# Kernel optimization log

Measured on AMD Instinct MI355X. Metric: run time of the kernel, lower is better.

## Reference

```python
import jax, jax.numpy as jnp
import numpy as np

N_NODES = 50000
N_EDGES = 400000
DIM = 64
HEADS = 8
NUM_GRAPHS = 64
OUT_DIM = 32
NEG_SLOPE = 0.2
EPS = 1e-5


def setup_inputs() -> dict:
    key = jax.random.key(0)
    ks = jax.random.split(key, 20)
    inp = {
        "x": jax.random.normal(ks[0], (N_NODES, DIM), dtype=jnp.float32),
        "edge_index": jax.random.randint(ks[1], (2, N_EDGES), 0, N_NODES, dtype=jnp.int64),
        "batch": jnp.sort(jax.random.randint(ks[2], (N_NODES,), 0, NUM_GRAPHS, dtype=jnp.int64)),
    }
    s = 0.05
    # GATConv layer 1 (in=DIM, out=DIM per head, heads=HEADS, concat=False)
    inp["W1"] = jax.random.normal(ks[3], (DIM, HEADS * DIM), dtype=jnp.float32) * s
    inp["a_src1"] = jax.random.normal(ks[4], (HEADS, DIM), dtype=jnp.float32) * s
    inp["a_dst1"] = jax.random.normal(ks[5], (HEADS, DIM), dtype=jnp.float32) * s
    inp["b1"] = jnp.zeros((DIM,), dtype=jnp.float32)
    inp["ln1_w"] = jnp.ones((DIM,), dtype=jnp.float32)
    inp["ln1_b"] = jnp.zeros((DIM,), dtype=jnp.float32)
    # GATConv layer 2
    inp["W2"] = jax.random.normal(ks[6], (DIM, HEADS * DIM), dtype=jnp.float32) * s
    inp["a_src2"] = jax.random.normal(ks[7], (HEADS, DIM), dtype=jnp.float32) * s
    inp["a_dst2"] = jax.random.normal(ks[8], (HEADS, DIM), dtype=jnp.float32) * s
    inp["b2"] = jnp.zeros((DIM,), dtype=jnp.float32)
    inp["ln2_w"] = jnp.ones((DIM,), dtype=jnp.float32)
    inp["ln2_b"] = jnp.zeros((DIM,), dtype=jnp.float32)
    # DownStream head
    inp["Wh"] = jax.random.normal(ks[9], (DIM, OUT_DIM), dtype=jnp.float32) * s
    inp["bh"] = jnp.zeros((OUT_DIM,), dtype=jnp.float32)
    return inp


def _edge_softmax(logits, dst, n):
    # per-destination-node softmax over incoming edges; logits: [E, H]
    m = jax.ops.segment_max(logits, dst, num_segments=n)
    e = jnp.exp(logits - m[dst])
    s = jax.ops.segment_sum(e, dst, num_segments=n)
    return e / (s[dst] + 1e-16)


def _gat_conv(x, src, dst, W, a_src, a_dst, b):
    # PyG GATConv, heads=HEADS, concat=False (mean over heads), eval mode (no dropout)
    n = x.shape[0]
    h = (x @ W).reshape(n, HEADS, -1)              # [N, H, D]
    al_s = jnp.einsum("nhd,hd->nh", h, a_src)      # [N, H]
    al_d = jnp.einsum("nhd,hd->nh", h, a_dst)
    logits = jax.nn.leaky_relu(al_s[src] + al_d[dst], NEG_SLOPE)  # [E, H]
    alpha = _edge_softmax(logits, dst, n)
    out = jax.ops.segment_sum(alpha[:, :, None] * h[src], dst, num_segments=n)  # [N, H, D]
    return out.mean(axis=1) + b


def _graph_layer_norm(x, batch, w, b):
    # PyG LayerNorm mode='graph': normalize over all nodes and channels of each graph
    f = x.shape[1]
    cnt = jax.ops.segment_sum(jnp.ones((x.shape[0],), x.dtype), batch, num_segments=NUM_GRAPHS)
    norm = jnp.clip(cnt, 1.0) * f
    mean = jax.ops.segment_sum(x.sum(axis=-1), batch, num_segments=NUM_GRAPHS) / norm
    xc = x - mean[batch][:, None]
    var = jax.ops.segment_sum((xc * xc).sum(axis=-1), batch, num_segments=NUM_GRAPHS) / norm
    out = xc * jax.lax.rsqrt(var + EPS)[batch][:, None]
    return out * w + b


def reference(x, edge_index, batch, W1, a_src1, a_dst1, b1, ln1_w, ln1_b,
              W2, a_src2, a_dst2, b2, ln2_w, ln2_b, Wh, bh):
    n = x.shape[0]
    loops = jnp.arange(n, dtype=edge_index.dtype)
    src = jnp.concatenate([edge_index[0], loops])   # add_self_loops (PyG default)
    dst = jnp.concatenate([edge_index[1], loops])

    # My_GATConv (dropout is identity in eval)
    h = x + _gat_conv(x, src, dst, W1, a_src1, a_dst1, b1)
    h = jax.nn.relu(_graph_layer_norm(h, batch, ln1_w, ln1_b))
    h = h + _gat_conv(h, src, dst, W2, a_src2, a_dst2, b2)
    h = jax.nn.relu(_graph_layer_norm(h, batch, ln2_w, ln2_b))

    # global_mean_pool over batch
    cnt = jax.ops.segment_sum(jnp.ones((n,), h.dtype), batch, num_segments=NUM_GRAPHS)
    pooled = jax.ops.segment_sum(h, batch, num_segments=NUM_GRAPHS) / jnp.clip(cnt, 1.0)[:, None]

    # DownStream head
    return jax.nn.relu(pooled @ Wh + bh)
```

## Files before the change

### kernel.cpp

```cpp
#include <hip/hip_runtime.h>
#include <math.h>

#define N_NODES 50000
#define N_EDGES 400000
#define E_TOT   (N_EDGES + N_NODES)
#define NG      64
#define NEG_SLOPE 0.2f

typedef __attribute__((ext_vector_type(8))) short bf16x8;
typedef __attribute__((ext_vector_type(4))) float f32x4;

__device__ __forceinline__ float lrelu(float x){ return x > 0.f ? x : NEG_SLOPE * x; }
__device__ __forceinline__ ushort f2bf(float f){
  union { float f; unsigned u; } v; v.f = f;
  unsigned r = v.u + 0x7FFFu + ((v.u >> 16) & 1u);
  return (ushort)(r >> 16);
}
__device__ __forceinline__ float bf2f(ushort u){
  return __uint_as_float(((unsigned)u) << 16);
}
__device__ __forceinline__ float bflo(unsigned u){ return __uint_as_float(u << 16); }
__device__ __forceinline__ float bfhi(unsigned u){ return __uint_as_float(u & 0xffff0000u); }

#define SETUP_PREP   (2048 + 2 * 32768)
#define SETUP_BOUNDS (SETUP_PREP + N_NODES + 1)
#define SETUP_TOTAL  (SETUP_BOUNDS + E_TOT)

__global__ void setup_kernel(const float* __restrict__ W1, const float* __restrict__ as1,
                             const float* __restrict__ ad1, const float* __restrict__ W2,
                             const float* __restrict__ as2, const float* __restrict__ ad2,
                             const int* __restrict__ batch, const int* __restrict__ ei,
                             float* __restrict__ wa1, float* __restrict__ wa2,
                             ushort* __restrict__ w1pT, ushort* __restrict__ w2pT,
                             int* __restrict__ gstart, int* __restrict__ counts){
  int idx = blockIdx.x * blockDim.x + threadIdx.x;
  if (idx < 2048){
    const float* W = (idx < 1024) ? W1 : W2;
    const float* asr = (idx < 1024) ? as1 : as2;
    const float* adr = (idx < 1024) ? ad1 : ad2;
    float* wa = (idx < 1024) ? wa1 : wa2;
    int i = idx & 1023;
    int k = i >> 4, c = i & 15;
    int h = c & 7;
    const float* a = (c < 8) ? asr : adr;
    float s = 0.f;
#pragma unroll
    for (int d = 0; d < 64; ++d) s = fmaf(W[k * 512 + h * 64 + d], a[h * 64 + d], s);
    wa[i] = s;
  } else if (idx < SETUP_PREP){
    int i = idx - 2048;
    const float* W = (i < 32768) ? W1 : W2;
    ushort* wpT = (i < 32768) ? w1pT : w2pT;
    i &= 32767;
    int j = i >> 9, k = i & 511;
    int d = k >> 3, h = k & 7;
    wpT[i] = f2bf(W[d * 512 + h * 64 + j] * 0.125f);
  } else if (idx < SETUP_BOUNDS){
    int n = idx - SETUP_PREP;
    int g = (n < N_NODES) ? batch[n] : NG;
    if (n == 0){
      for (int gg = 0; gg <= g; ++gg) gstart[gg] = 0;
    } else {
      int gp = batch[n - 1];
      for (int gg = gp + 1; gg <= g; ++gg) gstart[gg] = n;
    }
  } else if (idx < SETUP_TOTAL){
    int e = idx - SETUP_BOUNDS;
    int dst = (e < N_EDGES) ? ei[N_EDGES + e] : (e - N_EDGES);
    atomicAdd(&counts[dst], 1);
  }
}

#define SCAN_B 1024
#define SCAN_NB ((N_NODES + SCAN_B - 1) / SCAN_B)

__global__ __launch_bounds__(SCAN_B) void scan1_kernel(const int* __restrict__ counts,
                                                       int* __restrict__ row_off,
                                                       int* __restrict__ blocksum){
  __shared__ int sh[SCAN_B];
  int i = blockIdx.x * SCAN_B + threadIdx.x;
  int v = (i < N_NODES) ? counts[i] : 0;
  sh[threadIdx.x] = v;
  __syncthreads();
#pragma unroll
  for (int off = 1; off < SCAN_B; off <<= 1){
    int add = (threadIdx.x >= (unsigned)off) ? sh[threadIdx.x - off] : 0;
    __syncthreads();
    sh[threadIdx.x] += add;
    __syncthreads();
  }
  if (i < N_NODES) row_off[i] = sh[threadIdx.x] - v;
  if (threadIdx.x == SCAN_B - 1) blocksum[blockIdx.x] = sh[SCAN_B - 1];
}

__global__ void scan2_kernel(int* __restrict__ blocksum, int* __restrict__ blockoff){
  __shared__ int sh[64];
  int t = threadIdx.x;
  int v = (t < SCAN_NB) ? blocksum[t] : 0;
  sh[t] = v;
  __syncthreads();
#pragma unroll
  for (int off = 1; off < 64; off <<= 1){
    int add = (t >= off) ? sh[t - off] : 0;
    __syncthreads();
    sh[t] += add;
    __syncthreads();
  }
  if (t < SCAN_NB) blockoff[t] = sh[t] - v;
  if (t == 63) blockoff[SCAN_NB] = sh[63];
}

__global__ void scan3_kernel(int* __restrict__ row_off, const int* __restrict__ blockoff){
  int i = blockIdx.x * blockDim.x + threadIdx.x;
  if (i < N_NODES) row_off[i] += blockoff[i >> 10];
  if (i == 0) row_off[N_NODES] = blockoff[SCAN_NB];
}

__global__ void scatter_kernel(const int* __restrict__ ei, const int* __restrict__ row_off,
                               int* __restrict__ cursor, int* __restrict__ csr_src){
  int e = blockIdx.x * blockDim.x + threadIdx.x;
  if (e >= E_TOT) return;
  int src, dst;
  if (e < N_EDGES){ src = ei[e]; dst = ei[N_EDGES + e]; }
  else            { src = dst = e - N_EDGES; }
  int pos = row_off[dst] + atomicAdd(&cursor[dst], 1);
  csr_src[pos] = src;
}

__global__ void al1_kernel(const float* __restrict__ xin, const float* __restrict__ wa,
                           float* __restrict__ al, ushort* __restrict__ xbf){
  __shared__ float w[64 * 16];
  for (int i = threadIdx.x; i < 1024; i += blockDim.x) w[i] = wa[i];
  __syncthreads();
  int idx = blockIdx.x * blockDim.x + threadIdx.x;
  if (idx >= N_NODES * 16) return;
  int n = idx >> 4, c = idx & 15;
  const float* xr = xin + (size_t)n * 64;
  float s = 0.f;
#pragma unroll
  for (int k4 = 0; k4 < 16; ++k4){
    float4 v = *(const float4*)(xr + k4 * 4);
    s = fmaf(v.x, w[(k4 * 4 + 0) * 16 + c], s);
    s = fmaf(v.y, w[(k4 * 4 + 1) * 16 + c], s);
    s = fmaf(v.z, w[(k4 * 4 + 2) * 16 + c], s);
    s = fmaf(v.w, w[(k4 * 4 + 3) * 16 + c], s);
  }
  float4 mine = *(const float4*)(xr + c * 4);
  ushort ob[4] = {f2bf(mine.x), f2bf(mine.y), f2bf(mine.z), f2bf(mine.w)};
  *(ushort4*)(xbf + (size_t)n * 64 + c * 4) = *(const ushort4*)ob;
  al[idx] = s;
}

__global__ __launch_bounds__(256) void wagg_kernel(const ushort* __restrict__ xb,
                                                   const float* __restrict__ al,
                                                   const int* __restrict__ row_off,
                                                   const int* __restrict__ csr_src,
                                                   ushort* __restrict__ aggx){
  __shared__ float ws[4][64][8];
  __shared__ int sdeg[4];
  const int wave = threadIdx.x >> 6, lane = threadIdx.x & 63;
  const int n = blockIdx.x * 4 + wave;
  const int s0 = row_off[n], s1 = row_off[n + 1];
  const int deg = s1 - s0;
  if (lane == 0) sdeg[wave] = deg;
  __syncthreads();
  const int mdeg = max(max(sdeg[0], sdeg[1]), max(sdeg[2], sdeg[3]));
  const int nchunk = (mdeg + 63) >> 6;

  const int eo = lane >> 3, h = lane & 7;
  const float ald = al[n * 16 + 8 + h];

  int idxv = (s0 + lane < s1) ? csr_src[s0 + lane] : 0;

  const bool fast = (deg <= 64);
  float wv[8];
  float sum = 0.f;
  if (fast){
#pragma unroll
    for (int i = 0; i < 8; ++i){
      int ee = eo + i * 8;
      int s = __shfl(idxv, ee, 64);
      float v = 0.f;
      if (ee < deg) v = __expf(lrelu(al[s * 16 + h] + ald));
      wv[i] = v; sum += v;
    }
  } else {
    for (int e = s0 + eo; e < s1; e += 8){
      int s = csr_src[e];
      sum += __expf(lrelu(al[s * 16 + h] + ald));
    }
  }
#pragma unroll
  for (int off = 8; off < 64; off <<= 1) sum += __shfl_xor(sum, off, 64);
  const float inv = 1.f / (sum + 1e-16f);

  float acc[8];
#pragma unroll
  for (int i = 0; i < 8; ++i) acc[i] = 0.f;

  for (int c = 0; c < nchunk; ++c){
    const int base = s0 + c * 64;
    if (fast){
      if (c == 0){
#pragma unroll
        for (int i = 0; i < 8; ++i){
          int ee = eo + i * 8;
          if (ee < deg) ws[wave][ee][h] = wv[i] * inv;
        }
      }
    } else {
#pragma unroll
      for (int i = 0; i < 8; ++i){
        int e = base + eo + i * 8;
        if (e < s1){
          int s = csr_src[e];
          ws[wave][e - base][h] = __expf(lrelu(al[s * 16 + h] + ald)) * inv;
        }
      }
    }
    __syncthreads();
    const int cend = min(base + 64, s1);
    int e = base;
    for (; e + 4 <= cend; e += 4){
      int r0 = e - base;
      int sa, sb, sc, sd;
      if (fast){
        sa = __shfl(idxv, e - s0, 64);
        sb = __shfl(idxv, e - s0 + 1, 64);
        sc = __shfl(idxv, e - s0 + 2, 64);
        sd = __shfl(idxv, e - s0 + 3, 64);
      } else {
        sa = csr_src[e]; sb = csr_src[e + 1]; sc = csr_src[e + 2]; sd = csr_src[e + 3];
      }
      float xa = bf2f(xb[(size_t)sa * 64 + lane]);
      float xc = bf2f(xb[(size_t)sb * 64 + lane]);
      float xe = bf2f(xb[(size_t)sc * 64 + lane]);
      float xg = bf2f(xb[(size_t)sd * 64 + lane]);
      float4 wa0 = *(const float4*)&ws[wave][r0][0];
      float4 wa1 = *(const float4*)&ws[wave][r0][4];
      float4 wb0 = *(const float4*)&ws[wave][r0 + 1][0];
      float4 wb1 = *(const float4*)&ws[wave][r0 + 1][4];
      float4 wc0 = *(const float4*)&ws[wave][r0 + 2][0];
      float4 wc1 = *(const float4*)&ws[wave][r0 + 2][4];
      float4 wd0 = *(const float4*)&ws[wave][r0 + 3][0];
      float4 wd1 = *(const float4*)&ws[wave][r0 + 3][4];
      acc[0] = fmaf(wa0.x, xa, acc[0]); acc[1] = fmaf(wa0.y, xa, acc[1]);
      acc[2] = fmaf(wa0.z, xa, acc[2]); acc[3] = fmaf(wa0.w, xa, acc[3]);
      acc[4] = fmaf(wa1.x, xa, acc[4]); acc[5] = fmaf(wa1.y, xa, acc[5]);
      acc[6] = fmaf(wa1.z, xa, acc[6]); acc[7] = fmaf(wa1.w, xa, acc[7]);
      acc[0] = fmaf(wb0.x, xc, acc[0]); acc[1] = fmaf(wb0.y, xc, acc[1]);
      acc[2] = fmaf(wb0.z, xc, acc[2]); acc[3] = fmaf(wb0.w, xc, acc[3]);
      acc[4] = fmaf(wb1.x, xc, acc[4]); acc[5] = fmaf(wb1.y, xc, acc[5]);
      acc[6] = fmaf(wb1.z, xc, acc[6]); acc[7] = fmaf(wb1.w, xc, acc[7]);
      acc[0] = fmaf(wc0.x, xe, acc[0]); acc[1] = fmaf(wc0.y, xe, acc[1]);
      acc[2] = fmaf(wc0.z, xe, acc[2]); acc[3] = fmaf(wc0.w, xe, acc[3]);
      acc[4] = fmaf(wc1.x, xe, acc[4]); acc[5] = fmaf(wc1.y, xe, acc[5]);
      acc[6] = fmaf(wc1.z, xe, acc[6]); acc[7] = fmaf(wc1.w, xe, acc[7]);
      acc[0] = fmaf(wd0.x, xg, acc[0]); acc[1] = fmaf(wd0.y, xg, acc[1]);
      acc[2] = fmaf(wd0.z, xg, acc[2]); acc[3] = fmaf(wd0.w, xg, acc[3]);
      acc[4] = fmaf(wd1.x, xg, acc[4]); acc[5] = fmaf(wd1.y, xg, acc[5]);
      acc[6] = fmaf(wd1.z, xg, acc[6]); acc[7] = fmaf(wd1.w, xg, acc[7]);
    }
    for (; e < cend; ++e){
      int r0 = e - base;
      int sa = fast ? __shfl(idxv, e - s0, 64) : csr_src[e];
      float xa = bf2f(xb[(size_t)sa * 64 + lane]);
      float4 wa0 = *(const float4*)&ws[wave][r0][0];
      float4 wa1 = *(const float4*)&ws[wave][r0][4];
      acc[0] = fmaf(wa0.x, xa, acc[0]); acc[1] = fmaf(wa0.y, xa, acc[1]);
      acc[2] = fmaf(wa0.z, xa, acc[2]); acc[3] = fmaf(wa0.w, xa, acc[3]);
      acc[4] = fmaf(wa1.x, xa, acc[4]); acc[5] = fmaf(wa1.y, xa, acc[5]);
      acc[6] = fmaf(wa1.z, xa, acc[6]); acc[7] = fmaf(wa1.w, xa, acc[7]);
    }
    __syncthreads();
  }
  uint o[4];
#pragma unroll
  for (int i = 0; i < 4; ++i)
    o[i] = (uint)f2bf(acc[2 * i]) | ((uint)f2bf(acc[2 * i + 1]) << 16);
  *(uint4*)(aggx + (size_t)n * 512 + lane * 8) = make_uint4(o[0], o[1], o[2], o[3]);
}

__global__ __launch_bounds__(256) void outgemm_stats_kernel(const ushort* __restrict__ A,
                                                            const ushort* __restrict__ BT,
                                                            const float* __restrict__ bias,
                                                            const float* __restrict__ res,
                                                            const int* __restrict__ batch,
                                                            float* __restrict__ Y,
                                                            float* __restrict__ gs,
                                                            float* __restrict__ gss){
  __shared__ ushort Al[64][136];
  __shared__ ushort Bl[64][136];
  __shared__ float gsl[NG], gssl[NG];
  const int t = threadIdx.x;
  const int wave = t >> 6, lane = t & 63;
  const int rowbase = blockIdx.x * 64;
  const int frow = lane & 15, kc = lane >> 4;
  if (t < NG){ gsl[t] = 0.f; gssl[t] = 0.f; }
  f32x4 acc[4];
#pragma unroll
  for (int ct = 0; ct < 4; ++ct) acc[ct] = (f32x4){0.f, 0.f, 0.f, 0.f};

  for (int k0 = 0; k0 < 512; k0 += 128){
#pragma unroll
    for (int ppass = 0; ppass < 4; ++ppass){
      int idx = (ppass * 256 + t) * 8;
      int r = idx >> 7, k = idx & 127;
      int grow = rowbase + r;
      uint4 v = make_uint4(0u, 0u, 0u, 0u);
      if (grow < N_NODES) v = *(const uint4*)(A + (size_t)grow * 512 + k0 + k);
      *(uint4*)&Al[r][k] = v;
      uint4 w = *(const uint4*)(BT + (size_t)r * 512 + k0 + k);
      *(uint4*)&Bl[r][k] = w;
    }
    __syncthreads();
#pragma unroll
    for (int kf = 0; kf < 4; ++kf){
      bf16x8 a = *(const bf16x8*)&Al[wave * 16 + frow][kf * 32 + kc * 8];
#pragma unroll
      for (int ct = 0; ct < 4; ++ct){
        bf16x8 b = *(const bf16x8*)&Bl[ct * 16 + frow][kf * 32 + kc * 8];
        acc[ct] = __builtin_amdgcn_mfma_f32_16x16x32_bf16(a, b, acc[ct], 0, 0, 0);
      }
    }
    __syncthreads();
  }
  const int col0 = lane & 15, rsub = (lane >> 4) * 4;
  float rs[4] = {0.f, 0.f, 0.f, 0.f}, rss[4] = {0.f, 0.f, 0.f, 0.f};
#pragma unroll
  for (int ct = 0; ct < 4; ++ct){
    int col = ct * 16 + col0;
    float bs = bias[col];
#pragma unroll
    for (int j = 0; j < 4; ++j){
      int grow = rowbase + wave * 16 + rsub + j;
      if (grow < N_NODES){
        float y = acc[ct][j] + bs + res[(size_t)grow * 64 + col];
        Y[(size_t)grow * 64 + col] = y;
        rs[j] += y;
        rss[j] = fmaf(y, y, rss[j]);
      }
    }
  }
#pragma unroll
  for (int j = 0; j < 4; ++j){
#pragma unroll
    for (int off = 1; off < 16; off <<= 1){
      rs[j] += __shfl_xor(rs[j], off, 64);
      rss[j] += __shfl_xor(rss[j], off, 64);
    }
  }
  if (col0 == 0){
#pragma unroll
    for (int j = 0; j < 4; ++j){
      int grow = rowbase + wave * 16 + rsub + j;
      if (grow < N_NODES){
        int g = batch[grow];
        atomicAdd(&gsl[g], rs[j]);
        atomicAdd(&gssl[g], rss[j]);
      }
    }
  }
  __syncthreads();
  if (t < NG && (gsl[t] != 0.f || gssl[t] != 0.f)){
    atomicAdd(&gs[t], gsl[t]);
    atomicAdd(&gss[t], gssl[t]);
  }
}

__global__ __launch_bounds__(256) void norm_relu_al_kernel(const float* __restrict__ Y,
                                                           const int* __restrict__ batch,
                                                           const int* __restrict__ gstart,
                                                           const float* __restrict__ gs,
                                                           const float* __restrict__ gss,
                                                           const float* __restrict__ lw,
                                                           const float* __restrict__ lb,
                                                           const float* __restrict__ wa,
                                                           float* __restrict__ out,
                                                           ushort* __restrict__ outb,
                                                           float* __restrict__ al){
  __shared__ float rows[4][64];
  const int t = threadIdx.x;
  const int nl = t >> 6, c = t & 63;
  const int n = blockIdx.x * 4 + nl;
  int g = batch[n];
  float cnt = (float)(gstart[g + 1] - gstart[g]);
  float norm = fmaxf(cnt, 1.f) * 64.f;
  float m = gs[g] / norm;
  float var = fmaxf(gss[g] / norm - m * m, 0.f);
  float rstd = rsqrtf(var + 1e-5f);
  float v = (Y[(size_t)n * 64 + c] - m) * rstd * lw[c] + lb[c];
  float r = fmaxf(v, 0.f);
  out[(size_t)n * 64 + c] = r;
  outb[(size_t)n * 64 + c] = f2bf(r);
  rows[nl][c] = r;
  __syncthreads();
  if (t < 64){
    int nn = t >> 4, cc = t & 15;
    float s = 0.f;
#pragma unroll
    for (int k = 0; k < 64; ++k) s = fmaf(rows[nn][k], wa[k * 16 + cc], s);
    al[(size_t)(blockIdx.x * 4 + nn) * 16 + cc] = s;
  }
}

__global__ void norm_relu_pool_kernel(const float* __restrict__ Y, const int* __restrict__ batch,
                                      const int* __restrict__ gstart, const float* __restrict__ gs,
                                      const float* __restrict__ gss,
                                      const float* __restrict__ lw, const float* __restrict__ lb,
                                      float* __restrict__ pooled){
  int w = (int)((blockIdx.x * blockDim.x + threadIdx.x) >> 6);
  int lane = threadIdx.x & 63;
  int nbase = w * 16;
  if (nbase >= N_NODES) return;
  int nend = min(nbase + 16, N_NODES);
  float accv = 0.f;
  int g = batch[nbase];
  float cnt = (float)(gstart[g + 1] - gstart[g]);
  float norm = fmaxf(cnt, 1.f) * 64.f;
  float m = gs[g] / norm;
  float var = fmaxf(gss[g] / norm - m * m, 0.f);
  float rstd = rsqrtf(var + 1e-5f);
  for (int n = nbase; n < nend; ++n){
    int gn = batch[n];
    if (gn != g){
      atomicAdd(&pooled[g * 64 + lane], accv);
      accv = 0.f; g = gn;
      cnt = (float)(gstart[g + 1] - gstart[g]);
      norm = fmaxf(cnt, 1.f) * 64.f;
      m = gs[g] / norm;
      var = fmaxf(gss[g] / norm - m * m, 0.f);
      rstd = rsqrtf(var + 1e-5f);
    }
    float v = (Y[(size_t)n * 64 + lane] - m) * rstd * lw[lane] + lb[lane];
    accv += fmaxf(v, 0.f);
  }
  atomicAdd(&pooled[g * 64 + lane], accv);
}

__global__ void head_kernel(const float* __restrict__ pooled, const int* __restrict__ gstart,
                            const float* __restrict__ Wh, const float* __restrict__ bh,
                            float* __restrict__ out){
  int idx = blockIdx.x * blockDim.x + threadIdx.x;
  if (idx >= NG * 32) return;
  int g = idx >> 5, o = idx & 31;
  float cnt = (float)(gstart[g + 1] - gstart[g]);
  float inv = 1.f / fmaxf(cnt, 1.f);
  float s = 0.f;
#pragma unroll
  for (int d = 0; d < 64; ++d) s = fmaf(pooled[g * 64 + d] * inv, Wh[d * 32 + o], s);
  out[idx] = fmaxf(s + bh[o], 0.f);
}

extern "C" void kernel_launch(void* const* d_in, const int* in_sizes, int n_in,
                              void* d_out, int out_size, void* d_ws, size_t ws_size,
                              hipStream_t stream){
  const float* x     = (const float*)d_in[0];
  const int*   ei    = (const int*)d_in[1];
  const int*   batch = (const int*)d_in[2];
  const float* W1    = (const float*)d_in[3];
  const float* as1   = (const float*)d_in[4];
  const float* ad1   = (const float*)d_in[5];
  const float* b1    = (const float*)d_in[6];
  const float* l1w   = (const float*)d_in[7];
  const float* l1b   = (const float*)d_in[8];
  const float* W2    = (const float*)d_in[9];
  const float* as2   = (const float*)d_in[10];
  const float* ad2   = (const float*)d_in[11];
  const float* b2    = (const float*)d_in[12];
  const float* l2w   = (const float*)d_in[13];
  const float* l2b   = (const float*)d_in[14];
  const float* Wh    = (const float*)d_in[15];
  const float* bh    = (const float*)d_in[16];
  float* out = (float*)d_out;

  char* p = (char*)d_ws;
  auto alloc = [&](size_t bytes) -> void* {
    void* r = (void*)p;
    p += (bytes + 255) & ~(size_t)255;
    return r;
  };
  int*    counts   = (int*)alloc(N_NODES * 4);
  int*    cursor   = (int*)alloc(N_NODES * 4);
  int*    row_off  = (int*)alloc((N_NODES + 1) * 4);
  int*    csr_src  = (int*)alloc(E_TOT * 4);
  int*    gstart   = (int*)alloc((NG + 1) * 4);
  int*    blocksum = (int*)alloc((SCAN_NB + 1) * 4);
  int*    blockoff = (int*)alloc((SCAN_NB + 1) * 4);
  float*  wa1      = (float*)alloc(64 * 16 * 4);
  float*  wa2      = (float*)alloc(64 * 16 * 4);
  ushort* w1pT     = (ushort*)alloc(64 * 512 * 2);
  ushort* w2pT     = (ushort*)alloc(64 * 512 * 2);
  float*  al       = (float*)alloc((size_t)N_NODES * 16 * 4);
  ushort* xbf      = (ushort*)alloc((size_t)N_NODES * 64 * 2);
  ushort* y1b      = (ushort*)alloc((size_t)N_NODES * 64 * 2);
  ushort* aggx     = (ushort*)alloc((size_t)N_NODES * 512 * 2);
  float*  y1p      = (float*)alloc((size_t)N_NODES * 64 * 4);
  float*  y1       = (float*)alloc((size_t)N_NODES * 64 * 4);
  float*  y2p      = y1p;
  float*  gstats   = (float*)alloc(8 * NG * 4);
  float*  pooled   = (float*)alloc(NG * 64 * 4);
  float* gs1 = gstats, *gss1 = gstats + NG, *gs2 = gstats + 2*NG, *gss2 = gstats + 3*NG;

  hipMemsetAsync(counts, 0, (size_t)((char*)row_off - (char*)counts), stream);
  hipMemsetAsync(gstats, 0, (size_t)((char*)pooled - (char*)gstats) + NG * 64 * 4, stream);

  setup_kernel<<<(SETUP_TOTAL + 255) / 256, 256, 0, stream>>>(
      W1, as1, ad1, W2, as2, ad2, batch, ei, wa1, wa2, w1pT, w2pT, gstart, counts);

  scan1_kernel<<<SCAN_NB, SCAN_B, 0, stream>>>(counts, row_off, blocksum);
  scan2_kernel<<<1, 64, 0, stream>>>(blocksum, blockoff);
  scan3_kernel<<<(N_NODES + 255) / 256, 256, 0, stream>>>(row_off, blockoff);
  scatter_kernel<<<(E_TOT + 255) / 256, 256, 0, stream>>>(ei, row_off, cursor, csr_src);

  const int waggBlocks = N_NODES / 4;
  const int waveBlocks = ((N_NODES + 15) / 16 * 64 + 255) / 256;
  const int gemmBlocks = (N_NODES + 63) / 64;

  al1_kernel<<<(N_NODES * 16 + 255) / 256, 256, 0, stream>>>(x, wa1, al, xbf);
  wagg_kernel<<<waggBlocks, 256, 0, stream>>>(xbf, al, row_off, csr_src, aggx);
  outgemm_stats_kernel<<<gemmBlocks, 256, 0, stream>>>(aggx, w1pT, b1, x, batch, y1p, gs1, gss1);
  norm_relu_al_kernel<<<waggBlocks, 256, 0, stream>>>(y1p, batch, gstart, gs1, gss1, l1w, l1b, wa2, y1, y1b, al);

  wagg_kernel<<<waggBlocks, 256, 0, stream>>>(y1b, al, row_off, csr_src, aggx);
  outgemm_stats_kernel<<<gemmBlocks, 256, 0, stream>>>(aggx, w2pT, b2, y1, batch, y2p, gs2, gss2);
  norm_relu_pool_kernel<<<waveBlocks, 256, 0, stream>>>(y2p, batch, gstart, gs2, gss2, l2w, l2b, pooled);

  head_kernel<<<(NG * 32 + 255) / 256, 256, 0, stream>>>(pooled, gstart, Wh, bh, out);
}
```

Before: 231.9 us.

## Prefetch neighbor rows early, defer softmax normalization, use bf16 residuals

In the aggregation kernel, the first up-to-16 neighbor feature rows are loaded before the attention-weight computation so their gather latency overlaps the exp/sum work. The softmax normalization is moved to a single multiply of the accumulators at the end, which removes the register-held weight array and a second pass over the weights. The residual inputs to the output GEMM are now read from the existing bf16 copies instead of fp32 arrays, so the fp32 y1 buffer and its write are removed. This lowers memory traffic but adds bf16 rounding error to the residual path and raises register pressure from the prefetch array.

```diff
diff --git a/kernel.cpp b/kernel.cpp
--- a/kernel.cpp
+++ b/kernel.cpp
@@ -19,8 +19,6 @@
 __device__ __forceinline__ float bf2f(ushort u){
   return __uint_as_float(((unsigned)u) << 16);
 }
-__device__ __forceinline__ float bflo(unsigned u){ return __uint_as_float(u << 16); }
-__device__ __forceinline__ float bfhi(unsigned u){ return __uint_as_float(u & 0xffff0000u); }
 
 #define SETUP_PREP   (2048 + 2 * 32768)
 #define SETUP_BOUNDS (SETUP_PREP + N_NODES + 1)
@@ -157,6 +155,7 @@
                                                    const int* __restrict__ csr_src,
                                                    ushort* __restrict__ aggx){
   __shared__ float ws[4][64][8];
+  __shared__ float sinv[4][8];
   __shared__ int sdeg[4];
   const int wave = threadIdx.x >> 6, lane = threadIdx.x & 63;
   const int n = blockIdx.x * 4 + wave;
@@ -172,17 +171,28 @@
 
   int idxv = (s0 + lane < s1) ? csr_src[s0 + lane] : 0;
 
+  const int dpre = min(deg, 16);
+  float xpre[16];
+#pragma unroll
+  for (int i = 0; i < 16; ++i){
+    if (i < dpre){
+      int s = __shfl(idxv, i, 64);
+      xpre[i] = bf2f(xb[(size_t)s * 64 + lane]);
+    }
+  }
+
   const bool fast = (deg <= 64);
-  float wv[8];
   float sum = 0.f;
   if (fast){
 #pragma unroll
     for (int i = 0; i < 8; ++i){
       int ee = eo + i * 8;
       int s = __shfl(idxv, ee, 64);
-      float v = 0.f;
-      if (ee < deg) v = __expf(lrelu(al[s * 16 + h] + ald));
-      wv[i] = v; sum += v;
+      if (ee < deg){
+        float v = __expf(lrelu(al[s * 16 + h] + ald));
+        ws[wave][ee][h] = v;
+        sum += v;
+      }
     }
   } else {
     for (int e = s0 + eo; e < s1; e += 8){
@@ -192,7 +202,7 @@
   }
 #pragma unroll
   for (int off = 8; off < 64; off <<= 1) sum += __shfl_xor(sum, off, 64);
-  const float inv = 1.f / (sum + 1e-16f);
+  if (eo == 0) sinv[wave][h] = 1.f / (sum + 1e-16f);
 
   float acc[8];
 #pragma unroll
@@ -200,27 +210,34 @@
 
   for (int c = 0; c < nchunk; ++c){
     const int base = s0 + c * 64;
-    if (fast){
-      if (c == 0){
-#pragma unroll
-        for (int i = 0; i < 8; ++i){
-          int ee = eo + i * 8;
-          if (ee < deg) ws[wave][ee][h] = wv[i] * inv;
-        }
-      }
-    } else {
+    if (!fast){
 #pragma unroll
       for (int i = 0; i < 8; ++i){
         int e = base + eo + i * 8;
         if (e < s1){
           int s = csr_src[e];
-          ws[wave][e - base][h] = __expf(lrelu(al[s * 16 + h] + ald)) * inv;
+          ws[wave][e - base][h] = __expf(lrelu(al[s * 16 + h] + ald));
         }
       }
     }
     __syncthreads();
     const int cend = min(base + 64, s1);
     int e = base;
+    if (c == 0){
+#pragma unroll
+      for (int i = 0; i < 16; ++i){
+        if (i < dpre){
+          float4 w0 = *(const float4*)&ws[wave][i][0];
+          float4 w1 = *(const float4*)&ws[wave][i][4];
+          float xa = xpre[i];
+          acc[0] = fmaf(w0.x, xa, acc[0]); acc[1] = fmaf(w0.y, xa, acc[1]);
+          acc[2] = fmaf(w0.z, xa, acc[2]); acc[3] = fmaf(w0.w, xa, acc[3]);
+          acc[4] = fmaf(w1.x, xa, acc[4]); acc[5] = fmaf(w1.y, xa, acc[5]);
+          acc[6] = fmaf(w1.z, xa, acc[6]); acc[7] = fmaf(w1.w, xa, acc[7]);
+        }
+      }
+      e = base + dpre;
+    }
     for (; e + 4 <= cend; e += 4){
       int r0 = e - base;
       int sa, sb, sc, sd;
@@ -274,6 +291,10 @@
     }
     __syncthreads();
   }
+  float4 i0 = *(const float4*)&sinv[wave][0];
+  float4 i1 = *(const float4*)&sinv[wave][4];
+  acc[0] *= i0.x; acc[1] *= i0.y; acc[2] *= i0.z; acc[3] *= i0.w;
+  acc[4] *= i1.x; acc[5] *= i1.y; acc[6] *= i1.z; acc[7] *= i1.w;
   uint o[4];
 #pragma unroll
   for (int i = 0; i < 4; ++i)
@@ -284,7 +305,7 @@
 __global__ __launch_bounds__(256) void outgemm_stats_kernel(const ushort* __restrict__ A,
                                                             const ushort* __restrict__ BT,
                                                             const float* __restrict__ bias,
-                                                            const float* __restrict__ res,
+                                                            const ushort* __restrict__ res,
                                                             const int* __restrict__ batch,
                                                             float* __restrict__ Y,
                                                             float* __restrict__ gs,
@@ -335,7 +356,7 @@
     for (int j = 0; j < 4; ++j){
       int grow = rowbase + wave * 16 + rsub + j;
       if (grow < N_NODES){
-        float y = acc[ct][j] + bs + res[(size_t)grow * 64 + col];
+        float y = acc[ct][j] + bs + bf2f(res[(size_t)grow * 64 + col]);
         Y[(size_t)grow * 64 + col] = y;
         rs[j] += y;
         rss[j] = fmaf(y, y, rss[j]);
@@ -376,7 +397,6 @@
                                                            const float* __restrict__ lw,
                                                            const float* __restrict__ lb,
                                                            const float* __restrict__ wa,
-                                                           float* __restrict__ out,
                                                            ushort* __restrict__ outb,
                                                            float* __restrict__ al){
   __shared__ float rows[4][64];
@@ -391,7 +411,6 @@
   float rstd = rsqrtf(var + 1e-5f);
   float v = (Y[(size_t)n * 64 + c] - m) * rstd * lw[c] + lb[c];
   float r = fmaxf(v, 0.f);
-  out[(size_t)n * 64 + c] = r;
   outb[(size_t)n * 64 + c] = f2bf(r);
   rows[nl][c] = r;
   __syncthreads();
@@ -496,7 +515,6 @@
   ushort* y1b      = (ushort*)alloc((size_t)N_NODES * 64 * 2);
   ushort* aggx     = (ushort*)alloc((size_t)N_NODES * 512 * 2);
   float*  y1p      = (float*)alloc((size_t)N_NODES * 64 * 4);
-  float*  y1       = (float*)alloc((size_t)N_NODES * 64 * 4);
   float*  y2p      = y1p;
   float*  gstats   = (float*)alloc(8 * NG * 4);
   float*  pooled   = (float*)alloc(NG * 64 * 4);
@@ -519,11 +537,11 @@
 
   al1_kernel<<<(N_NODES * 16 + 255) / 256, 256, 0, stream>>>(x, wa1, al, xbf);
   wagg_kernel<<<waggBlocks, 256, 0, stream>>>(xbf, al, row_off, csr_src, aggx);
-  outgemm_stats_kernel<<<gemmBlocks, 256, 0, stream>>>(aggx, w1pT, b1, x, batch, y1p, gs1, gss1);
-  norm_relu_al_kernel<<<waggBlocks, 256, 0, stream>>>(y1p, batch, gstart, gs1, gss1, l1w, l1b, wa2, y1, y1b, al);
+  outgemm_stats_kernel<<<gemmBlocks, 256, 0, stream>>>(aggx, w1pT, b1, xbf, batch, y1p, gs1, gss1);
+  norm_relu_al_kernel<<<waggBlocks, 256, 0, stream>>>(y1p, batch, gstart, gs1, gss1, l1w, l1b, wa2, y1b, al);
 
   wagg_kernel<<<waggBlocks, 256, 0, stream>>>(y1b, al, row_off, csr_src, aggx);
-  outgemm_stats_kernel<<<gemmBlocks, 256, 0, stream>>>(aggx, w2pT, b2, y1, batch, y2p, gs2, gss2);
+  outgemm_stats_kernel<<<gemmBlocks, 256, 0, stream>>>(aggx, w2pT, b2, y1b, batch, y2p, gs2, gss2);
   norm_relu_pool_kernel<<<waveBlocks, 256, 0, stream>>>(y2p, batch, gstart, gs2, gss2, l2w, l2b, pooled);
 
   head_kernel<<<(NG * 32 + 255) / 256, 256, 0, stream>>>(pooled, gstart, Wh, bh, out);
```

Result: slower. 489.6 us (+111.1%).
